# Kernel optimization log

Measured on AMD Instinct MI355X. Metric: run time of the kernel, lower is better.

## Reference

```python
import jax, jax.numpy as jnp
import numpy as np

E = 1024   # embed_dim
H = 1024   # hidden_dim
NH = 16    # num_heads
HD = H // NH
B, P, C = 2, 1024, 1024


def _layernorm(x, g, b):
    m = jnp.mean(x, axis=-1, keepdims=True)
    v = jnp.mean((x - m) ** 2, axis=-1, keepdims=True)
    return (x - m) / jnp.sqrt(v + 1e-5) * g + b


def _attention(problem, context, Wq, bq, Wk, bk, Wv, bv, mask, num_heads, head_dim, head_out_dim):
    # Faithful to source: head axis LAST in the reshape, mask added AFTER softmax.
    batch = problem.shape[0]
    q = (problem @ Wq + bq).reshape(batch, -1, head_dim, num_heads)      # b i d h
    k = (context @ Wk + bk).reshape(batch, -1, head_dim, num_heads)      # b j d h
    v = (context @ Wv + bv).reshape(batch, -1, head_out_dim, num_heads)  # b j o h
    scores = jnp.einsum('bidh,bjdh->bijh', q, k) / jnp.sqrt(jnp.asarray(head_dim, q.dtype))
    p = jax.nn.softmax(scores, axis=2)
    if mask is not None:
        p = p + mask[..., None]
    out = jnp.einsum('bijh,bjoh->bioh', p, v)
    return out.reshape(batch, -1, head_out_dim * num_heads)


def setup_inputs() -> dict:
    key = jax.random.key(0)
    ks = jax.random.split(key, 20)
    s = 0.02
    inp = {
        'x': jax.random.normal(ks[0], (B, P, E), jnp.float32),
        'context': jax.random.normal(ks[1], (B, C, E), jnp.float32),
        'causal_mask': jnp.zeros((B, P, P), jnp.float32),
        'problem_pad_mask': jnp.zeros((B, P, P), jnp.float32),
        'context_pad_mask': jnp.zeros((B, P, C), jnp.float32),
        # self-attn params (out_dim = E)
        'sa_Wq': jax.random.normal(ks[2], (E, H), jnp.float32) * s, 'sa_bq': jnp.zeros((H,), jnp.float32),
        'sa_Wk': jax.random.normal(ks[3], (E, H), jnp.float32) * s, 'sa_bk': jnp.zeros((H,), jnp.float32),
        'sa_Wv': jax.random.normal(ks[4], (E, E), jnp.float32) * s, 'sa_bv': jnp.zeros((E,), jnp.float32),
        # cross-attn params
        'ca_Wq': jax.random.normal(ks[5], (E, H), jnp.float32) * s, 'ca_bq': jnp.zeros((H,), jnp.float32),
        'ca_Wk': jax.random.normal(ks[6], (E, H), jnp.float32) * s, 'ca_bk': jnp.zeros((H,), jnp.float32),
        'ca_Wv': jax.random.normal(ks[7], (E, E), jnp.float32) * s, 'ca_bv': jnp.zeros((E,), jnp.float32),
        # layernorms
        'ln1_g': jnp.ones((E,), jnp.float32), 'ln1_b': jnp.zeros((E,), jnp.float32),
        'ln2_g': jnp.ones((E,), jnp.float32), 'ln2_b': jnp.zeros((E,), jnp.float32),
        'ln3_g': jnp.ones((E,), jnp.float32), 'ln3_b': jnp.zeros((E,), jnp.float32),
        # mlp
        'mlp_W1': jax.random.normal(ks[8], (E, H), jnp.float32) * s, 'mlp_b1': jnp.zeros((H,), jnp.float32),
        'mlp_W2': jax.random.normal(ks[9], (H, E), jnp.float32) * s, 'mlp_b2': jnp.zeros((E,), jnp.float32),
    }
    return inp


def reference(x, context, causal_mask, problem_pad_mask, context_pad_mask,
              sa_Wq, sa_bq, sa_Wk, sa_bk, sa_Wv, sa_bv,
              ca_Wq, ca_bq, ca_Wk, ca_bk, ca_Wv, ca_bv,
              ln1_g, ln1_b, ln2_g, ln2_b, ln3_g, ln3_b,
              mlp_W1, mlp_b1, mlp_W2, mlp_b2):
    self_attn_mask = causal_mask + problem_pad_mask
    xc = x
    x = _attention(x, x, sa_Wq, sa_bq, sa_Wk, sa_bk, sa_Wv, sa_bv, self_attn_mask, NH, HD, E // NH)
    x = _layernorm(x, ln1_g, ln1_b) + xc
    xc = x
    x = _attention(x, context, ca_Wq, ca_bq, ca_Wk, ca_bk, ca_Wv, ca_bv, context_pad_mask, NH, HD, E // NH)
    x = _layernorm(x, ln2_g, ln2_b) + xc
    xc = x
    x = jax.nn.relu(x @ mlp_W1 + mlp_b1) @ mlp_W2 + mlp_b2
    return _layernorm(x, ln3_g, ln3_b) + xc
```

## Files before the change

### kernel.cpp

```cpp
#include <hip/hip_runtime.h>
#include <math.h>

#define NHEADS 16

typedef __attribute__((ext_vector_type(8))) short bf16x8;
typedef __attribute__((ext_vector_type(4))) float f32x4;

__device__ inline short f2b(float f) {
  unsigned u = __float_as_uint(f);
  u += 0x7fffu + ((u >> 16) & 1u);
  return (short)(u >> 16);
}
__device__ inline float b2f(short s) {
  return __uint_as_float(((unsigned)(unsigned short)s) << 16);
}
__device__ inline void gld16(const void* g, void* l) {
  __builtin_amdgcn_global_load_lds(
      (const __attribute__((address_space(1))) unsigned int*)g,
      (__attribute__((address_space(3))) unsigned int*)l, 16, 0, 0);
}
#define MFMA16(a, b, c) __builtin_amdgcn_mfma_f32_16x16x32_bf16(a, b, c, 0, 0, 0)

__global__ __launch_bounds__(256) void prep_wt(
    const float* __restrict__ x, const float* __restrict__ ctx,
    const float* __restrict__ cm, const float* __restrict__ ppm,
    const float* __restrict__ cpm,
    const float* sabq, const float* sabk, const float* sabv,
    const float* cabk, const float* cabv, const float* cabq,
    const float* W0, const float* W1, const float* W2, const float* W3,
    const float* W4, const float* W5, const float* W6, const float* W7,
    short* __restrict__ XB, short* __restrict__ CTXB,
    short* __restrict__ MBSA, short* __restrict__ MBCA,
    float* __restrict__ qkvb, float* __restrict__ kvb,
    float* __restrict__ qpb, unsigned* __restrict__ kmaxu,
    short* __restrict__ WT) {
  __shared__ float t[64][65];
  const int blk = blockIdx.x;
  const int tid = threadIdx.x;
  const int n4 = 2048 * 1024 / 4;
  if (blk < 8192) {
    int seg = blk >> 11;
    int i = (blk & 2047) * 256 + tid;
    if (i >= n4) return;
    float4 va;
    short* out;
    if (seg == 0) { va = ((const float4*)x)[i]; out = XB; }
    else if (seg == 1) { va = ((const float4*)ctx)[i]; out = CTXB; }
    else if (seg == 2) {
      va = ((const float4*)cm)[i];
      float4 vb = ((const float4*)ppm)[i];
      va.x += vb.x; va.y += vb.y; va.z += vb.z; va.w += vb.w;
      out = MBSA;
    } else { va = ((const float4*)cpm)[i]; out = MBCA; }
    short4 s;
    s.x = f2b(va.x); s.y = f2b(va.y); s.z = f2b(va.z); s.w = f2b(va.w);
    ((short4*)out)[i] = s;
    return;
  }
  if (blk < 8216) {
    if (blk == 8192 && tid < 64) kmaxu[tid] = 0u;
    int i = (blk - 8192) * 256 + tid;
    if (i >= 6144) return;
    int j = i & 1023;
    int pj = ((j & 63) << 4) | (j >> 6);
    int sec = i >> 10;
    if (sec == 0) qkvb[j] = sabq[pj];
    else if (sec == 1) qkvb[1024 + j] = sabk[pj];
    else if (sec == 2) qkvb[2048 + j] = sabv[pj];
    else if (sec == 3) kvb[j] = cabk[pj];
    else if (sec == 4) kvb[1024 + j] = cabv[pj];
    else qpb[j] = cabq[pj];
    return;
  }
  const int blk2 = blk - 8216;
  const int wz = blk2 >> 8;
  const int rem = blk2 & 255;
  const float* W;
  switch (wz) {
    case 0: W = W0; break; case 1: W = W1; break;
    case 2: W = W2; break; case 3: W = W3; break;
    case 4: W = W4; break; case 5: W = W5; break;
    case 6: W = W6; break; default: W = W7; break;
  }
  const int permute = (wz < 6) ? 1 : 0;
  short* o = WT + (size_t)wz * 1024 * 1024;
  const int n0 = (rem & 15) * 64, k0 = (rem >> 4) * 64;
  const int cg = (tid & 15) * 4, rg = tid >> 4;
  #pragma unroll
  for (int r = 0; r < 4; ++r) {
    int kl = rg + r * 16;
    float4 v = *(const float4*)(W + (size_t)(k0 + kl) * 1024 + n0 + cg);
    t[kl][cg + 0] = v.x; t[kl][cg + 1] = v.y;
    t[kl][cg + 2] = v.z; t[kl][cg + 3] = v.w;
  }
  __syncthreads();
  #pragma unroll
  for (int r = 0; r < 4; ++r) {
    int nl = rg + r * 16;
    int n = n0 + nl;
    int nrow = permute ? (((n & 15) << 6) | (n >> 4)) : n;
    short4 s;
    s.x = f2b(t[cg + 0][nl]); s.y = f2b(t[cg + 1][nl]);
    s.z = f2b(t[cg + 2][nl]); s.w = f2b(t[cg + 3][nl]);
    *(short4*)(o + (size_t)nrow * 1024 + k0 + cg) = s;
  }
}

template <int TN>
__global__ __launch_bounds__(256) void gemmT(
    const short* __restrict__ A, const short* __restrict__ Bt,
    const float* __restrict__ bias,
    void* __restrict__ C0, short* __restrict__ C1, short* __restrict__ C2,
    int mode, int relu, int ny,
    const short* __restrict__ A2, const short* __restrict__ Bt2,
    const float* __restrict__ bias2,
    void* __restrict__ D0, short* __restrict__ D1, short* __restrict__ D2,
    int mode2, int relu2, int ny2,
    unsigned* __restrict__ kout) {
  if (blockIdx.z == 1) {
    A = A2; Bt = Bt2; bias = bias2;
    C0 = D0; C1 = D1; C2 = D2; mode = mode2; relu = relu2; ny = ny2;
  }
  if ((int)blockIdx.y >= ny) return;

  constexpr int NT = TN / 32;
  constexpr int BR = TN / 4;
  __shared__ short As[64 * 64];
  __shared__ short Bs[TN * 64];
  const int tid = threadIdx.x;
  const int w = tid >> 6, l = tid & 63;
  const int ln = l & 15, lq = l >> 4;
  const int wm = w >> 1, wn = w & 1;
  const int m0 = blockIdx.x * 64, n0 = blockIdx.y * TN;
  const int K = 1024;

  f32x4 acc[2][NT];
  #pragma unroll
  for (int s = 0; s < 2; ++s)
    #pragma unroll
    for (int t = 0; t < NT; ++t) acc[s][t] = (f32x4){0.f, 0.f, 0.f, 0.f};

  const int srow = l >> 3;
  const int sch = (l & 7) ^ srow;
  const short* ga = A + (size_t)(m0 + w * 16 + srow) * K + sch * 8;
  const short* gb = Bt + (size_t)(n0 + w * BR + srow) * K + sch * 8;
  short* la = &As[w * 16 * 64];
  short* lb = &Bs[w * BR * 64];

  for (int k0 = 0; k0 < K; k0 += 64) {
    __syncthreads();
    gld16(ga + k0, la);
    gld16(ga + (size_t)8 * K + k0, la + 512);
    #pragma unroll
    for (int rb = 0; rb < BR / 8; ++rb)
      gld16(gb + (size_t)rb * 8 * K + k0, lb + rb * 512);
    __syncthreads();
    #pragma unroll
    for (int kc = 0; kc < 2; ++kc) {
      const int co = ((kc * 4 + lq) ^ (ln & 7)) * 8;
      bf16x8 af[2], bf[NT];
      af[0] = *(const bf16x8*)&As[(wm * 32 + ln) * 64 + co];
      af[1] = *(const bf16x8*)&As[(wm * 32 + 16 + ln) * 64 + co];
      #pragma unroll
      for (int t = 0; t < NT; ++t)
        bf[t] = *(const bf16x8*)&Bs[(wn * (TN / 2) + t * 16 + ln) * 64 + co];
      #pragma unroll
      for (int s = 0; s < 2; ++s)
        #pragma unroll
        for (int t = 0; t < NT; ++t)
          acc[s][t] = MFMA16(af[s], bf[t], acc[s][t]);
    }
  }

  float bv[NT];
  #pragma unroll
  for (int t = 0; t < NT; ++t) bv[t] = bias[n0 + wn * (TN / 2) + t * 16 + ln];

  #pragma unroll
  for (int s = 0; s < 2; ++s) {
    #pragma unroll
    for (int t = 0; t < NT; ++t) {
      #pragma unroll
      for (int r = 0; r < 4; ++r) {
        int m = m0 + wm * 32 + s * 16 + lq * 4 + r;
        int n = n0 + wn * (TN / 2) + t * 16 + ln;
        float v = acc[s][t][r] + bv[t];
        if (relu) v = fmaxf(v, 0.f);
        int bb = m >> 10, ii = m & 1023;
        if (mode == 0) {
          ((float*)C0)[(size_t)m * 1024 + n] = v;
        } else if (mode == 1) {
          ((short*)C0)[(size_t)m * 1024 + n] = f2b(v);
        } else if (mode == 2) {
          int hh = n >> 6, d = n & 63;
          ((short*)C0)[(((size_t)(bb * 16 + hh)) * 1024 + ii) * 64 + d] = f2b(v);
        } else if (mode == 3) {
          int sel = n >> 10, g = n & 1023;
          int hh = g >> 6, d = g & 63;
          if (sel == 0)
            ((short*)C0)[(((size_t)(bb * 16 + hh)) * 1024 + ii) * 64 + d] = f2b(v);
          else if (sel == 1)
            C1[(((size_t)(bb * 16 + hh)) * 1024 + ii) * 64 + d] = f2b(v);
          else
            C2[(((size_t)(bb * 16 + hh)) * 64 + d) * 1024 + ii] = f2b(v);
        } else {
          int sel = n >> 10, g = n & 1023;
          int hh = g >> 6, d = g & 63;
          if (sel == 0)
            C1[(((size_t)(bb * 16 + hh)) * 1024 + ii) * 64 + d] = f2b(v);
          else
            C2[(((size_t)(bb * 16 + hh)) * 64 + d) * 1024 + ii] = f2b(v);
        }
      }
    }
  }

  if constexpr (TN == 128) {
    const int nb = n0 + wn * 64;
    const int selw = nb >> 10;
    if ((mode == 3 && selw == 1) || (mode == 4 && selw == 0)) {
      const int slotbase = (mode == 3) ? 0 : 32;
      const int bb = m0 >> 10;
      const int hh = (nb & 1023) >> 6;
      float mx = 0.f;
      #pragma unroll
      for (int s = 0; s < 2; ++s)
        #pragma unroll
        for (int r = 0; r < 4; ++r) {
          float ss = 0.f;
          #pragma unroll
          for (int t = 0; t < 4; ++t) {
            float v = acc[s][t][r] + bv[t];
            ss += v * v;
          }
          ss += __shfl_xor(ss, 1, 64);
          ss += __shfl_xor(ss, 2, 64);
          ss += __shfl_xor(ss, 4, 64);
          ss += __shfl_xor(ss, 8, 64);
          mx = fmaxf(mx, ss);
        }
      mx = fmaxf(mx, __shfl_xor(mx, 16, 64));
      mx = fmaxf(mx, __shfl_xor(mx, 32, 64));
      if (l == 0)
        atomicMax(kout + slotbase + bb * 16 + hh, __float_as_uint(mx));
    }
  }
}

__global__ __launch_bounds__(256) void attn_flash(
    const short* __restrict__ qh, const short* __restrict__ kh,
    const short* __restrict__ vt, const short* __restrict__ maskb,
    const unsigned* __restrict__ kmax, short* __restrict__ out) {
  __shared__ short Ks[128 * 64];
  __shared__ short Vs[64 * 128];
  __shared__ short Msk[64 * 128];
  __shared__ short Ps[4][16 * 72];
  __shared__ float Ml[64];
  const int tid = threadIdx.x;
  const int w = tid >> 6, l = tid & 63;
  const int ln = l & 15, lq = l >> 4;
  const int i0 = blockIdx.x * 64;
  const int b = blockIdx.z;
  const int bh = b * 16 + blockIdx.y;
  const size_t bho = (size_t)bh * 65536;

  const short* qp = qh + bho + (size_t)(i0 + w * 16 + ln) * 64 + lq * 8;
  bf16x8 qf0 = *(const bf16x8*)qp;
  bf16x8 qf1 = *(const bf16x8*)(qp + 32);

  float ssq = 0.f;
  #pragma unroll
  for (int e = 0; e < 8; ++e) {
    float f0 = b2f(qf0[e]), f1 = b2f(qf1[e]);
    ssq += f0 * f0 + f1 * f1;
  }
  ssq += __shfl_xor(ssq, 16, 64);
  ssq += __shfl_xor(ssq, 32, 64);
  float km = sqrtf(__uint_as_float(kmax[bh])) * 1.005f;
  if (lq == 0) Ml[w * 16 + ln] = sqrtf(ssq) * km * 0.125f + 1e-3f;
  float Mr[4], lac[4];
  #pragma unroll
  for (int r = 0; r < 4; ++r) { Mr[r] = Ml[w * 16 + lq * 4 + r]; lac[r] = 0.f; }

  const int r8 = l >> 3;
  const int c8 = (l & 7) ^ r8;
  const int r4 = l >> 4;
  const int cva = (l & 15) ^ r4;
  const short* gkb = kh + bho + (size_t)(w * 32 + r8) * 64 + c8 * 8;
  const short* gvb = vt + bho + (size_t)(w * 16 + r4) * 1024;
  const short* gmb = maskb + ((size_t)(b * 1024 + i0 + w * 16 + r4)) * 1024;
  short* lkb = &Ks[w * 32 * 64];
  short* lvb = &Vs[w * 16 * 128];
  short* lmb = &Msk[w * 16 * 128];
  short* PsW = &Ps[w][0];

  f32x4 oa[4], mo[4];
  #pragma unroll
  for (int os = 0; os < 4; ++os) {
    oa[os] = (f32x4){0.f, 0.f, 0.f, 0.f};
    mo[os] = (f32x4){0.f, 0.f, 0.f, 0.f};
  }

  const int c0 = (lq ^ (ln & 7)) * 8;
  const int c1 = ((4 | lq) ^ (ln & 7)) * 8;

  for (int jt = 0; jt < 8; ++jt) {
    const int j0 = jt * 128;
    __syncthreads();
    #pragma unroll
    for (int gi = 0; gi < 4; ++gi)
      gld16(gkb + (size_t)(j0 + gi * 8) * 64, lkb + gi * 512);
    #pragma unroll
    for (int gi = 0; gi < 4; ++gi) {
      int cc = (cva ^ ((gi & 1) << 2)) * 8;
      gld16(gvb + (size_t)gi * 4096 + j0 + cc, lvb + gi * 512);
      gld16(gmb + (size_t)gi * 4096 + j0 + cc, lmb + gi * 512);
    }
    __syncthreads();

    #pragma unroll
    for (int jh = 0; jh < 2; ++jh) {
      f32x4 sa[4];
      #pragma unroll
      for (int js = 0; js < 4; ++js) {
        const short* kr = &Ks[(jh * 64 + js * 16 + ln) * 64];
        bf16x8 kb0 = *(const bf16x8*)(kr + c0);
        bf16x8 kb1 = *(const bf16x8*)(kr + c1);
        f32x4 s = (f32x4){0.f, 0.f, 0.f, 0.f};
        s = MFMA16(qf0, kb0, s);
        s = MFMA16(qf1, kb1, s);
        sa[js] = s;
      }
      #pragma unroll
      for (int js = 0; js < 4; ++js)
        #pragma unroll
        for (int r = 0; r < 4; ++r) {
          float p = __expf(sa[js][r] * 0.125f - Mr[r]);
          lac[r] += p;
          PsW[(lq * 4 + r) * 72 + js * 16 + ln] = f2b(p);
        }
      bf16x8 pa0 = *(const bf16x8*)&PsW[ln * 72 + lq * 8];
      bf16x8 pa1 = *(const bf16x8*)&PsW[ln * 72 + 32 + lq * 8];
      const short* mr2 = &Msk[(w * 16 + ln) * 128 + jh * 64];
      bf16x8 ma0 = *(const bf16x8*)(mr2 + c0);
      bf16x8 ma1 = *(const bf16x8*)(mr2 + c1);
      #pragma unroll
      for (int os = 0; os < 4; ++os) {
        const short* vr = &Vs[(os * 16 + ln) * 128 + jh * 64];
        bf16x8 vb0 = *(const bf16x8*)(vr + c0);
        bf16x8 vb1 = *(const bf16x8*)(vr + c1);
        oa[os] = MFMA16(pa0, vb0, oa[os]);
        oa[os] = MFMA16(pa1, vb1, oa[os]);
        mo[os] = MFMA16(ma0, vb0, mo[os]);
        mo[os] = MFMA16(ma1, vb1, mo[os]);
      }
    }
  }

  #pragma unroll
  for (int r = 0; r < 4; ++r) {
    lac[r] += __shfl_xor(lac[r], 1, 64);
    lac[r] += __shfl_xor(lac[r], 2, 64);
    lac[r] += __shfl_xor(lac[r], 4, 64);
    lac[r] += __shfl_xor(lac[r], 8, 64);
  }
  float inv[4];
  #pragma unroll
  for (int r = 0; r < 4; ++r) inv[r] = 1.f / lac[r];

  #pragma unroll
  for (int os = 0; os < 4; ++os)
    #pragma unroll
    for (int r = 0; r < 4; ++r) {
      int row = i0 + w * 16 + lq * 4 + r;
      int o = os * 16 + ln;
      out[bho + (size_t)row * 64 + o] = f2b(oa[os][r] * inv[r] + mo[os][r]);
    }
}

__global__ __launch_bounds__(256) void ln_kernel(
    const void* __restrict__ xin, const short* __restrict__ res,
    const float* __restrict__ g, const float* __restrict__ be,
    void* __restrict__ outp, int out_bf16, int inmode) {
  const int row = blockIdx.x;
  const int tid = threadIdx.x;
  float4 v;
  if (inmode == 0) {
    v = ((const float4*)((const float*)xin + (size_t)row * 1024))[tid];
  } else if (inmode == 1) {
    int b = row >> 10, i = row & 1023;
    const short* base = (const short*)xin + (size_t)b * 16 * 65536 +
                        (size_t)i * 64;
    int o = tid >> 2, h0 = (tid & 3) * 4;
    v.x = b2f(base[(size_t)(h0 + 0) * 65536 + o]);
    v.y = b2f(base[(size_t)(h0 + 1) * 65536 + o]);
    v.z = b2f(base[(size_t)(h0 + 2) * 65536 + o]);
    v.w = b2f(base[(size_t)(h0 + 3) * 65536 + o]);
  } else {
    short4 s4 = ((const short4*)((const short*)xin + (size_t)row * 1024))[tid];
    v.x = b2f(s4.x); v.y = b2f(s4.y); v.z = b2f(s4.z); v.w = b2f(s4.w);
  }
  float s = v.x + v.y + v.z + v.w;
  float sq = v.x * v.x + v.y * v.y + v.z * v.z + v.w * v.w;
  #pragma unroll
  for (int off = 32; off > 0; off >>= 1) {
    s += __shfl_down(s, off, 64);
    sq += __shfl_down(sq, off, 64);
  }
  __shared__ float rs[4], rq[4], stat[2];
  int wave = tid >> 6, lane = tid & 63;
  if (lane == 0) { rs[wave] = s; rq[wave] = sq; }
  __syncthreads();
  if (tid == 0) {
    float S = rs[0] + rs[1] + rs[2] + rs[3];
    float Q = rq[0] + rq[1] + rq[2] + rq[3];
    float mean = S * (1.f / 1024.f);
    float var = Q * (1.f / 1024.f) - mean * mean;
    stat[0] = mean;
    stat[1] = rsqrtf(var + 1e-5f);
  }
  __syncthreads();
  float mean = stat[0], rstd = stat[1];
  float4 g4 = ((const float4*)g)[tid];
  float4 b4 = ((const float4*)be)[tid];
  short4 r4 = ((const short4*)(res + (size_t)row * 1024))[tid];
  float o0 = (v.x - mean) * rstd * g4.x + b4.x + b2f(r4.x);
  float o1 = (v.y - mean) * rstd * g4.y + b4.y + b2f(r4.y);
  float o2 = (v.z - mean) * rstd * g4.z + b4.z + b2f(r4.z);
  float o3 = (v.w - mean) * rstd * g4.w + b4.w + b2f(r4.w);
  if (out_bf16) {
    short4 o;
    o.x = f2b(o0); o.y = f2b(o1); o.z = f2b(o2); o.w = f2b(o3);
    ((short4*)outp)[(size_t)row * 256 + tid] = o;
  } else {
    float4 o = {o0, o1, o2, o3};
    ((float4*)outp)[(size_t)row * 256 + tid] = o;
  }
}

extern "C" void kernel_launch(void* const* d_in, const int* in_sizes, int n_in,
                              void* d_out, int out_size, void* d_ws, size_t ws_size,
                              hipStream_t stream) {
  const float* x    = (const float*)d_in[0];
  const float* ctx  = (const float*)d_in[1];
  const float* cm   = (const float*)d_in[2];
  const float* ppm  = (const float*)d_in[3];
  const float* cpm  = (const float*)d_in[4];
  const float* saWq = (const float*)d_in[5];
  const float* sabq = (const float*)d_in[6];
  const float* saWk = (const float*)d_in[7];
  const float* sabk = (const float*)d_in[8];
  const float* saWv = (const float*)d_in[9];
  const float* sabv = (const float*)d_in[10];
  const float* caWq = (const float*)d_in[11];
  const float* cabq = (const float*)d_in[12];
  const float* caWk = (const float*)d_in[13];
  const float* cabk = (const float*)d_in[14];
  const float* caWv = (const float*)d_in[15];
  const float* cabv = (const float*)d_in[16];
  const float* ln1g = (const float*)d_in[17];
  const float* ln1b = (const float*)d_in[18];
  const float* ln2g = (const float*)d_in[19];
  const float* ln2b = (const float*)d_in[20];
  const float* ln3g = (const float*)d_in[21];
  const float* ln3b = (const float*)d_in[22];
  const float* W1   = (const float*)d_in[23];
  const float* b1   = (const float*)d_in[24];
  const float* W2   = (const float*)d_in[25];
  const float* b2   = (const float*)d_in[26];

  char* ws = (char*)d_ws;
  const size_t MB = 1024 * 1024;
  short* WT       = (short*)(ws);
  float* qkvb     = (float*)(ws + 16 * MB);
  float* kvb      = (float*)(ws + 16 * MB + 16384);
  float* qpb      = (float*)(ws + 16 * MB + 32768);
  unsigned* kmaxu = (unsigned*)(ws + 16 * MB + 49152);
  short* MBSA  = (short*)(ws + 17 * MB);
  short* MBCA  = (short*)(ws + 21 * MB);
  short* XB    = (short*)(ws + 25 * MB);
  short* CTXB  = (short*)(ws + 29 * MB);
  short* QH    = (short*)(ws + 33 * MB);
  short* KH    = (short*)(ws + 37 * MB);
  short* VT    = (short*)(ws + 41 * MB);
  short* S3B   = (short*)(ws + 45 * MB);
  short* X1B   = (short*)(ws + 53 * MB);
  short* X2B   = MBSA;
  short* HB    = CTXB;
  float* outp  = (float*)d_out;

  dim3 lg(2048);
  const short* dsp = nullptr;
  const float* dfp = nullptr;

  prep_wt<<<dim3(10264), 256, 0, stream>>>(
      x, ctx, cm, ppm, cpm, sabq, sabk, sabv, cabk, cabv, cabq,
      saWq, saWk, saWv, caWk, caWv, caWq, W1, W2,
      XB, CTXB, MBSA, MBCA, qkvb, kvb, qpb, kmaxu, WT);

  gemmT<128><<<dim3(32, 24, 1), 256, 0, stream>>>(
      XB, WT, qkvb, QH, KH, VT, 3, 0, 24,
      dsp, dsp, dfp, nullptr, nullptr, nullptr, 0, 0, 0, kmaxu);

  attn_flash<<<dim3(16, 16, 2), 256, 0, stream>>>(QH, KH, VT, MBSA, kmaxu, S3B);
  ln_kernel<<<lg, 256, 0, stream>>>(S3B, XB, ln1g, ln1b, X1B, 1, 1);

  gemmT<128><<<dim3(32, 16, 2), 256, 0, stream>>>(
      X1B, WT + 5 * 1048576, qpb, QH, nullptr, nullptr, 2, 0, 8,
      CTXB, WT + 3 * 1048576, kvb, nullptr, KH, VT, 4, 0, 16, kmaxu);

  attn_flash<<<dim3(16, 16, 2), 256, 0, stream>>>(QH, KH, VT, MBCA,
                                                  kmaxu + 32, S3B);
  ln_kernel<<<lg, 256, 0, stream>>>(S3B, X1B, ln2g, ln2b, X2B, 1, 1);

  gemmT<64><<<dim3(32, 16, 1), 256, 0, stream>>>(
      X2B, WT + 6 * 1048576, b1, HB, nullptr, nullptr, 1, 1, 16,
      dsp, dsp, dfp, nullptr, nullptr, nullptr, 0, 0, 0, kmaxu);
  gemmT<64><<<dim3(32, 16, 1), 256, 0, stream>>>(
      HB, WT + 7 * 1048576, b2, S3B, nullptr, nullptr, 1, 0, 16,
      dsp, dsp, dfp, nullptr, nullptr, nullptr, 0, 0, 0, kmaxu);
  ln_kernel<<<lg, 256, 0, stream>>>(S3B, X2B, ln3g, ln3b, outp, 0, 2);
}
```

Measured before the change: 297.5 us.

## Skip all-zero mask MFMAs and overlap cross-attn KV GEMM with self-attention

Prep now ORs the mask bits into per-mask flags, and attention skips the mask loads and the mask·V MFMAs when the mask is entirely zero. This is a runtime data check, so the full computation still runs for nonzero masks. The cross-attention K/V projection of the context moves into extra z-slices of the self-attention launch, so it runs alongside attention and writes to new buffers. The cross Q GEMM becomes its own launch with a narrower tile, and a small init kernel clears the kmax and flag slots. Costs are an added atomic reduction in prep, one extra launch, and attention blocks that now mix GEMM and attention work.

```diff
diff --git a/kernel.cpp b/kernel.cpp
--- a/kernel.cpp
+++ b/kernel.cpp
@@ -20,6 +20,10 @@
       (__attribute__((address_space(3))) unsigned int*)l, 16, 0, 0);
 }
 #define MFMA16(a, b, c) __builtin_amdgcn_mfma_f32_16x16x32_bf16(a, b, c, 0, 0, 0)
+
+__global__ __launch_bounds__(128) void initk(unsigned* __restrict__ p) {
+  if (threadIdx.x < 66) p[threadIdx.x] = 0u;
+}
 
 __global__ __launch_bounds__(256) void prep_wt(
     const float* __restrict__ x, const float* __restrict__ ctx,
@@ -32,7 +36,7 @@
     short* __restrict__ XB, short* __restrict__ CTXB,
     short* __restrict__ MBSA, short* __restrict__ MBCA,
     float* __restrict__ qkvb, float* __restrict__ kvb,
-    float* __restrict__ qpb, unsigned* __restrict__ kmaxu,
+    float* __restrict__ qpb, unsigned* __restrict__ mflags,
     short* __restrict__ WT) {
   __shared__ float t[64][65];
   const int blk = blockIdx.x;
@@ -55,10 +59,17 @@
     short4 s;
     s.x = f2b(va.x); s.y = f2b(va.y); s.z = f2b(va.z); s.w = f2b(va.w);
     ((short4*)out)[i] = s;
+    if (seg >= 2) {
+      unsigned ob = __float_as_uint(va.x) | __float_as_uint(va.y) |
+                    __float_as_uint(va.z) | __float_as_uint(va.w);
+      #pragma unroll
+      for (int off = 1; off < 64; off <<= 1)
+        ob |= (unsigned)__shfl_xor((int)ob, off, 64);
+      if ((tid & 63) == 0 && ob) atomicOr(mflags + (seg - 2), ob);
+    }
     return;
   }
   if (blk < 8216) {
-    if (blk == 8192 && tid < 64) kmaxu[tid] = 0u;
     int i = (blk - 8192) * 256 + tid;
     if (i >= 6144) return;
     int j = i & 1023;
@@ -107,31 +118,19 @@
 }
 
 template <int TN>
-__global__ __launch_bounds__(256) void gemmT(
+__device__ __forceinline__ void gemm_core(
     const short* __restrict__ A, const short* __restrict__ Bt,
     const float* __restrict__ bias,
     void* __restrict__ C0, short* __restrict__ C1, short* __restrict__ C2,
-    int mode, int relu, int ny,
-    const short* __restrict__ A2, const short* __restrict__ Bt2,
-    const float* __restrict__ bias2,
-    void* __restrict__ D0, short* __restrict__ D1, short* __restrict__ D2,
-    int mode2, int relu2, int ny2,
-    unsigned* __restrict__ kout) {
-  if (blockIdx.z == 1) {
-    A = A2; Bt = Bt2; bias = bias2;
-    C0 = D0; C1 = D1; C2 = D2; mode = mode2; relu = relu2; ny = ny2;
-  }
-  if ((int)blockIdx.y >= ny) return;
-
+    int mode, int relu, int bx, int by,
+    unsigned* __restrict__ kout, short* As, short* Bs) {
   constexpr int NT = TN / 32;
   constexpr int BR = TN / 4;
-  __shared__ short As[64 * 64];
-  __shared__ short Bs[TN * 64];
   const int tid = threadIdx.x;
   const int w = tid >> 6, l = tid & 63;
   const int ln = l & 15, lq = l >> 4;
   const int wm = w >> 1, wn = w & 1;
-  const int m0 = blockIdx.x * 64, n0 = blockIdx.y * TN;
+  const int m0 = bx * 64, n0 = by * TN;
   const int K = 1024;
 
   f32x4 acc[2][NT];
@@ -247,22 +246,58 @@
   }
 }
 
+template <int TN>
+__global__ __launch_bounds__(256) void gemmT(
+    const short* __restrict__ A, const short* __restrict__ Bt,
+    const float* __restrict__ bias,
+    void* __restrict__ C0, short* __restrict__ C1, short* __restrict__ C2,
+    int mode, int relu, int ny,
+    const short* __restrict__ A2, const short* __restrict__ Bt2,
+    const float* __restrict__ bias2,
+    void* __restrict__ D0, short* __restrict__ D1, short* __restrict__ D2,
+    int mode2, int relu2, int ny2,
+    unsigned* __restrict__ kout) {
+  __shared__ short As[64 * 64];
+  __shared__ short Bs[TN * 64];
+  if (blockIdx.z == 1) {
+    A = A2; Bt = Bt2; bias = bias2;
+    C0 = D0; C1 = D1; C2 = D2; mode = mode2; relu = relu2; ny = ny2;
+  }
+  if ((int)blockIdx.y >= ny) return;
+  gemm_core<TN>(A, Bt, bias, C0, C1, C2, mode, relu, blockIdx.x, blockIdx.y,
+                kout, As, Bs);
+}
+
 __global__ __launch_bounds__(256) void attn_flash(
     const short* __restrict__ qh, const short* __restrict__ kh,
     const short* __restrict__ vt, const short* __restrict__ maskb,
-    const unsigned* __restrict__ kmax, short* __restrict__ out) {
+    const unsigned* __restrict__ kmax, short* __restrict__ out,
+    const unsigned* __restrict__ mflagp,
+    const short* __restrict__ gA, const short* __restrict__ gBt,
+    const float* __restrict__ gbias, short* __restrict__ gC1,
+    short* __restrict__ gC2, unsigned* __restrict__ gkout) {
   __shared__ short Ks[128 * 64];
   __shared__ short Vs[64 * 128];
   __shared__ short Msk[64 * 128];
   __shared__ short Ps[4][16 * 72];
   __shared__ float Ml[64];
+
+  const int z = blockIdx.z;
+  if (z >= 2) {
+    int gid = (z - 2) * 256 + blockIdx.y * 16 + blockIdx.x;
+    gemm_core<128>(gA, gBt, gbias, nullptr, gC1, gC2, 4, 0,
+                   gid & 31, gid >> 5, gkout, (short*)Ks, (short*)Vs);
+    return;
+  }
+
   const int tid = threadIdx.x;
   const int w = tid >> 6, l = tid & 63;
   const int ln = l & 15, lq = l >> 4;
   const int i0 = blockIdx.x * 64;
-  const int b = blockIdx.z;
+  const int b = z;
   const int bh = b * 16 + blockIdx.y;
   const size_t bho = (size_t)bh * 65536;
+  const unsigned mflag = *mflagp;
 
   const short* qp = qh + bho + (size_t)(i0 + w * 16 + ln) * 64 + lq * 8;
   bf16x8 qf0 = *(const bf16x8*)qp;
@@ -314,7 +349,13 @@
     for (int gi = 0; gi < 4; ++gi) {
       int cc = (cva ^ ((gi & 1) << 2)) * 8;
       gld16(gvb + (size_t)gi * 4096 + j0 + cc, lvb + gi * 512);
-      gld16(gmb + (size_t)gi * 4096 + j0 + cc, lmb + gi * 512);
+    }
+    if (mflag) {
+      #pragma unroll
+      for (int gi = 0; gi < 4; ++gi) {
+        int cc = (cva ^ ((gi & 1) << 2)) * 8;
+        gld16(gmb + (size_t)gi * 4096 + j0 + cc, lmb + gi * 512);
+      }
     }
     __syncthreads();
 
@@ -341,9 +382,6 @@
         }
       bf16x8 pa0 = *(const bf16x8*)&PsW[ln * 72 + lq * 8];
       bf16x8 pa1 = *(const bf16x8*)&PsW[ln * 72 + 32 + lq * 8];
-      const short* mr2 = &Msk[(w * 16 + ln) * 128 + jh * 64];
-      bf16x8 ma0 = *(const bf16x8*)(mr2 + c0);
-      bf16x8 ma1 = *(const bf16x8*)(mr2 + c1);
       #pragma unroll
       for (int os = 0; os < 4; ++os) {
         const short* vr = &Vs[(os * 16 + ln) * 128 + jh * 64];
@@ -351,8 +389,19 @@
         bf16x8 vb1 = *(const bf16x8*)(vr + c1);
         oa[os] = MFMA16(pa0, vb0, oa[os]);
         oa[os] = MFMA16(pa1, vb1, oa[os]);
-        mo[os] = MFMA16(ma0, vb0, mo[os]);
-        mo[os] = MFMA16(ma1, vb1, mo[os]);
+      }
+      if (mflag) {
+        const short* mr2 = &Msk[(w * 16 + ln) * 128 + jh * 64];
+        bf16x8 ma0 = *(const bf16x8*)(mr2 + c0);
+        bf16x8 ma1 = *(const bf16x8*)(mr2 + c1);
+        #pragma unroll
+        for (int os = 0; os < 4; ++os) {
+          const short* vr = &Vs[(os * 16 + ln) * 128 + jh * 64];
+          bf16x8 vb0 = *(const bf16x8*)(vr + c0);
+          bf16x8 vb1 = *(const bf16x8*)(vr + c1);
+          mo[os] = MFMA16(ma0, vb0, mo[os]);
+          mo[os] = MFMA16(ma1, vb1, mo[os]);
+        }
       }
     }
   }
@@ -476,6 +525,7 @@
   float* kvb      = (float*)(ws + 16 * MB + 16384);
   float* qpb      = (float*)(ws + 16 * MB + 32768);
   unsigned* kmaxu = (unsigned*)(ws + 16 * MB + 49152);
+  unsigned* mflags = kmaxu + 64;
   short* MBSA  = (short*)(ws + 17 * MB);
   short* MBCA  = (short*)(ws + 21 * MB);
   short* XB    = (short*)(ws + 25 * MB);
@@ -485,6 +535,8 @@
   short* VT    = (short*)(ws + 41 * MB);
   short* S3B   = (short*)(ws + 45 * MB);
   short* X1B   = (short*)(ws + 53 * MB);
+  short* KH2   = (short*)(ws + 57 * MB);
+  short* VT2   = (short*)(ws + 61 * MB);
   short* X2B   = MBSA;
   short* HB    = CTXB;
   float* outp  = (float*)d_out;
@@ -493,24 +545,31 @@
   const short* dsp = nullptr;
   const float* dfp = nullptr;
 
+  initk<<<dim3(1), 128, 0, stream>>>(kmaxu);
+
   prep_wt<<<dim3(10264), 256, 0, stream>>>(
       x, ctx, cm, ppm, cpm, sabq, sabk, sabv, cabk, cabv, cabq,
       saWq, saWk, saWv, caWk, caWv, caWq, W1, W2,
-      XB, CTXB, MBSA, MBCA, qkvb, kvb, qpb, kmaxu, WT);
+      XB, CTXB, MBSA, MBCA, qkvb, kvb, qpb, mflags, WT);
 
   gemmT<128><<<dim3(32, 24, 1), 256, 0, stream>>>(
       XB, WT, qkvb, QH, KH, VT, 3, 0, 24,
       dsp, dsp, dfp, nullptr, nullptr, nullptr, 0, 0, 0, kmaxu);
 
-  attn_flash<<<dim3(16, 16, 2), 256, 0, stream>>>(QH, KH, VT, MBSA, kmaxu, S3B);
+  attn_flash<<<dim3(16, 16, 4), 256, 0, stream>>>(
+      QH, KH, VT, MBSA, kmaxu, S3B, mflags,
+      CTXB, WT + 3 * 1048576, kvb, KH2, VT2, kmaxu);
+
   ln_kernel<<<lg, 256, 0, stream>>>(S3B, XB, ln1g, ln1b, X1B, 1, 1);
 
-  gemmT<128><<<dim3(32, 16, 2), 256, 0, stream>>>(
-      X1B, WT + 5 * 1048576, qpb, QH, nullptr, nullptr, 2, 0, 8,
-      CTXB, WT + 3 * 1048576, kvb, nullptr, KH, VT, 4, 0, 16, kmaxu);
-
-  attn_flash<<<dim3(16, 16, 2), 256, 0, stream>>>(QH, KH, VT, MBCA,
-                                                  kmaxu + 32, S3B);
+  gemmT<64><<<dim3(32, 16, 1), 256, 0, stream>>>(
+      X1B, WT + 5 * 1048576, qpb, QH, nullptr, nullptr, 2, 0, 16,
+      dsp, dsp, dfp, nullptr, nullptr, nullptr, 0, 0, 0, kmaxu);
+
+  attn_flash<<<dim3(16, 16, 2), 256, 0, stream>>>(
+      QH, KH2, VT2, MBCA, kmaxu + 32, S3B, mflags + 1,
+      dsp, dsp, dfp, nullptr, nullptr, kmaxu);
+
   ln_kernel<<<lg, 256, 0, stream>>>(S3B, X1B, ln2g, ln2b, X2B, 1, 1);
 
   gemmT<64><<<dim3(32, 16, 1), 256, 0, stream>>>(
@@ -519,5 +578,6 @@
   gemmT<64><<<dim3(32, 16, 1), 256, 0, stream>>>(
       HB, WT + 7 * 1048576, b2, S3B, nullptr, nullptr, 1, 0, 16,
       dsp, dsp, dfp, nullptr, nullptr, nullptr, 0, 0, 0, kmaxu);
+
   ln_kernel<<<lg, 256, 0, stream>>>(S3B, X2B, ln3g, ln3b, outp, 0, 2);
 }
```

After: 301.9 us. Within noise of the previous version (+1.5%).
